# Kernel tuning notes

Hardware: AMD Instinct MI355X
Metric: run time of the kernel (lower is better)

## Reference

```python
import jax, jax.numpy as jnp
import numpy as np

KS = 3      # deform/standard conv kernel size
PAD = 1     # padding == dilation == 1
EPS = 1e-5  # BatchNorm eps


def conv2d(x, w, b, stride=1, padding=0):
    out = jax.lax.conv_general_dilated(
        x, w, (stride, stride), [(padding, padding), (padding, padding)],
        dimension_numbers=('NCHW', 'OIHW', 'NCHW'))
    return out + b[None, :, None, None]


def bn_relu(x, bn):
    gamma, beta, mean, var = bn[0], bn[1], bn[2], bn[3]
    inv = gamma / jnp.sqrt(var + EPS)
    y = x * inv[None, :, None, None] + (beta - mean * inv)[None, :, None, None]
    return jax.nn.relu(y)


def _gather(xp_flat, qx, qy, Wp, c):
    # xp_flat: (b, c, Hp*Wp); qx, qy: (b, h, w, N) int32 -> (b, c, h, w, N)
    b = qx.shape[0]
    idx = (qx * Wp + qy).reshape(b, 1, -1)
    out = jnp.take_along_axis(xp_flat, jnp.broadcast_to(idx, (b, c, idx.shape[-1])), axis=2)
    return out.reshape(b, c, *qx.shape[1:])


def deform_conv(x, w_off, b_off, w_def, b_def, stride=1):
    b, c, H, W = x.shape
    N = KS * KS
    offset = conv2d(x, w_off, b_off, stride=stride, padding=1)  # (b, 2N, h, w)
    h, w = offset.shape[2], offset.shape[3]
    xp = jnp.pad(x, ((0, 0), (0, 0), (PAD, PAD), (PAD, PAD)))
    Hp, Wp = H + 2 * PAD, W + 2 * PAD
    r = (KS - 1) // 2
    pn_x, pn_y = jnp.meshgrid(jnp.arange(-r, r + 1), jnp.arange(-r, r + 1), indexing='ij')
    p_n = jnp.concatenate([pn_x.ravel(), pn_y.ravel()]).astype(x.dtype)  # (2N,)
    p0_x = jnp.arange(1, h * stride + 1, stride, dtype=x.dtype)
    p0_y = jnp.arange(1, w * stride + 1, stride, dtype=x.dtype)
    p0 = jnp.concatenate([jnp.broadcast_to(p0_x[None, :, None], (N, h, w)),
                          jnp.broadcast_to(p0_y[None, None, :], (N, h, w))], 0)
    p = (offset + p_n[None, :, None, None] + p0[None]).transpose(0, 2, 3, 1)  # (b,h,w,2N)
    q = jnp.floor(jax.lax.stop_gradient(p))
    lt_x = jnp.clip(q[..., :N], 0, Hp - 1); lt_y = jnp.clip(q[..., N:], 0, Wp - 1)
    rb_x = jnp.clip(q[..., :N] + 1, 0, Hp - 1); rb_y = jnp.clip(q[..., N:] + 1, 0, Wp - 1)
    p_x = jnp.clip(p[..., :N], 0, Hp - 1); p_y = jnp.clip(p[..., N:], 0, Wp - 1)
    g_lt = (1 + (lt_x - p_x)) * (1 + (lt_y - p_y))
    g_rb = (1 - (rb_x - p_x)) * (1 - (rb_y - p_y))
    g_lb = (1 + (lt_x - p_x)) * (1 - (rb_y - p_y))
    g_rt = (1 - (rb_x - p_x)) * (1 + (lt_y - p_y))
    xpf = xp.reshape(b, c, -1)
    ii = lambda t: t.astype(jnp.int32)
    x_lt = _gather(xpf, ii(lt_x), ii(lt_y), Wp, c)
    x_rb = _gather(xpf, ii(rb_x), ii(rb_y), Wp, c)
    x_lb = _gather(xpf, ii(lt_x), ii(rb_y), Wp, c)
    x_rt = _gather(xpf, ii(rb_x), ii(lt_y), Wp, c)
    x_off = (g_lt[:, None] * x_lt + g_rb[:, None] * x_rb +
             g_lb[:, None] * x_lb + g_rt[:, None] * x_rt)  # (b, c, h, w, N)
    # (b,c,h,w,ks_i,ks_j) -> (b,c,h*ks,w*ks), N ordered row-major (i*ks+j)
    x_off = x_off.reshape(b, c, h, w, KS, KS).transpose(0, 1, 2, 4, 3, 5).reshape(b, c, h * KS, w * KS)
    return conv2d(x_off, w_def, b_def, stride=KS, padding=0)


def setup_inputs() -> dict:
    key = jax.random.key(0)
    ks = jax.random.split(key, 16)
    B, Cin, H, W = 4, 128, 96, 96
    C2, Cout = 128, 256
    s = 0.05
    bn = lambda k1, k2: jnp.stack([jnp.ones(C2, jnp.float32), jnp.zeros(C2, jnp.float32),
                                   jax.random.normal(k1, (C2,)) * 0.1,
                                   jax.random.uniform(k2, (C2,)) + 0.5])
    return {
        'x': jax.random.normal(ks[0], (B, Cin, H, W), jnp.float32),
        'w_in': jax.random.normal(ks[1], (C2, Cin, 1, 1)) * s,
        'b_in': jax.random.normal(ks[2], (C2,)) * s,
        'w_off': jax.random.normal(ks[3], (2 * KS * KS, C2, 3, 3)) * s,
        'b_off': jax.random.normal(ks[4], (2 * KS * KS,)) * s,
        'w_def': jax.random.normal(ks[5], (C2, C2, KS, KS)) * s,
        'b_def': jax.random.normal(ks[6], (C2,)) * s,
        'bn1': bn(ks[7], ks[8]),
        'w_std': jax.random.normal(ks[9], (C2, C2, 3, 3)) * s,
        'b_std': jax.random.normal(ks[10], (C2,)) * s,
        'bn2': bn(ks[11], ks[12]),
        'w_out': jax.random.normal(ks[13], (Cout, Cout, 1, 1)) * s,
        'b_out': jax.random.normal(ks[14], (Cout,)) * s,
    }


def reference(x, w_in, b_in, w_off, b_off, w_def, b_def, bn1, w_std, b_std, bn2, w_out, b_out):
    x_c = conv2d(x, w_in, b_in)                                    # 1x1 reduce to ch_out/2
    x1 = bn_relu(deform_conv(x_c, w_off, b_off, w_def, b_def), bn1)  # deformable branch
    x2 = bn_relu(conv2d(x_c, w_std, b_std, padding=1), bn2)       # standard 3x3 branch
    # stride == 1 path: concat(deform, std + residual) then 1x1 fuse
    return conv2d(jnp.concatenate([x1, x2 + x_c], axis=1), w_out, b_out)
```

## Files before the change

### kernel.cpp

```cpp
#include <hip/hip_runtime.h>
#include <hip/hip_bf16.h>

#define BB 4
#define CC 128
#define HH 96
#define WW 96
#define PX (HH*WW)
#define HP 98
#define WP 98
#define PP (HP*WP)
#define K2 1152
#define BN_EPS 1e-5f

typedef __hip_bfloat16 bf16;
typedef __attribute__((ext_vector_type(8))) short bf16x8;
typedef __attribute__((ext_vector_type(4))) float f32x4;
__device__ __forceinline__ float b2f(bf16 v) { return __bfloat162float(v); }
union F8 { bf16x8 v; bf16 h[8]; int4 i4; };

#define MFMA(a, b, c) __builtin_amdgcn_mfma_f32_16x16x32_bf16((a), (b), (c), 0, 0, 0)

__device__ __forceinline__ float ldin(const void* p, size_t i, int f) {
  return f ? ((const float*)p)[i] : b2f(((const bf16*)p)[i]);
}

#define P_BIN  0
#define P_BOFF 128
#define P_BDEF 160
#define P_BN1  288
#define P_BSTD 800
#define P_BN2  928
#define P_BOUT 1440

__global__ __launch_bounds__(256) void probe_params(
    const void* bn1, const void* b_in, const void* b_off, const void* b_def,
    const void* b_std, const void* bn2, const void* b_out,
    int* __restrict__ flag, float* __restrict__ prm) {
  int f = (((const unsigned*)bn1)[0] == 0x3F800000u) ? 1 : 0;
  if (threadIdx.x == 0) flag[0] = f;
  int t = threadIdx.x;
  if (t < 128) prm[P_BIN + t]  = ldin(b_in, t, f);
  if (t < 18)  prm[P_BOFF + t] = ldin(b_off, t, f);
  if (t < 128) prm[P_BDEF + t] = ldin(b_def, t, f);
  for (int i = t; i < 512; i += 256) prm[P_BN1 + i] = ldin(bn1, i, f);
  if (t < 128) prm[P_BSTD + t] = ldin(b_std, t, f);
  for (int i = t; i < 512; i += 256) prm[P_BN2 + i] = ldin(bn2, i, f);
  if (t < 256) prm[P_BOUT + t] = ldin(b_out, t, f);
}

__global__ __launch_bounds__(256) void prep_weights(
    const void* w_in, const void* w_def, const void* w_std, const void* w_out,
    const void* w_off,
    bf16* __restrict__ w_inB, bf16* __restrict__ w_defB,
    bf16* __restrict__ w_stdB, bf16* __restrict__ w_outB,
    bf16* __restrict__ w_offP, const int* __restrict__ flag) {
  int f = flag[0];
  int i = blockIdx.x * 256 + threadIdx.x;
  if (i < K2 * 128) {
    int o = i / K2, kk = i - o * K2;
    int c = kk / 9, n = kk - c * 9;
    int dst = o * K2 + n * 128 + c;
    w_defB[dst] = __float2bfloat16(ldin(w_def, i, f));
    w_stdB[dst] = __float2bfloat16(ldin(w_std, i, f));
  }
  if (i < 32 * K2) {
    int o = i / K2, kk = i - o * K2;
    int c = kk / 9, n = kk - c * 9;
    int dst = o * K2 + n * 128 + c;
    w_offP[dst] = (o < 18) ? __float2bfloat16(ldin(w_off, i, f))
                           : __float2bfloat16(0.f);
  }
  if (i < 128 * 128) w_inB[i]  = __float2bfloat16(ldin(w_in, i, f));
  if (i < 256 * 256) w_outB[i] = __float2bfloat16(ldin(w_out, i, f));
}

__global__ __launch_bounds__(256) void conv1x1_in(
    const void* __restrict__ x, const bf16* __restrict__ wB,
    const float* __restrict__ prm, bf16* __restrict__ xcT,
    const int* __restrict__ flag, int b0) {
  __shared__ bf16 ct[128][136];
  bf16 (*xt)[40] = (bf16(*)[40])ct;
  int f = flag[0];
  int tid = threadIdx.x;
  int p0 = blockIdx.x * 128;
  int bg = b0 + blockIdx.y, bl = blockIdx.y;
  int lane = tid & 63, wv = tid >> 6;
  int quad = lane >> 4, l16 = lane & 15;
  int krow = tid >> 3, pxs = (tid & 7) * 16;
  int sgrp = (tid & 7) & 3;
  f32x4 acc[2][8] = {};
  for (int k0 = 0; k0 < 128; k0 += 32) {
    union { bf16 h[16]; int4 i4[2]; } u;
    size_t base = (size_t)(bg * 128 + k0 + krow) * PX + p0 + pxs;
    if (f) {
      const float4* s = (const float4*)((const float*)x + base);
#pragma unroll
      for (int v = 0; v < 4; ++v) {
        float4 t = s[v];
        u.h[v * 4 + 0] = __float2bfloat16(t.x);
        u.h[v * 4 + 1] = __float2bfloat16(t.y);
        u.h[v * 4 + 2] = __float2bfloat16(t.z);
        u.h[v * 4 + 3] = __float2bfloat16(t.w);
      }
    } else {
      const int4* s = (const int4*)((const bf16*)x + base);
      u.i4[0] = s[0]; u.i4[1] = s[1];
    }
    int col = (((krow >> 3) ^ sgrp) << 3) | (krow & 7);
    __syncthreads();
#pragma unroll
    for (int j = 0; j < 16; ++j) xt[pxs + j][col] = u.h[j];
    __syncthreads();
    const bf16* wp = wB + (size_t)(wv * 32 + l16) * 128 + k0 + quad * 8;
    bf16x8 a0 = *(const bf16x8*)wp;
    bf16x8 a1 = *(const bf16x8*)(wp + 16 * 128);
#pragma unroll
    for (int p = 0; p < 8; ++p) {
      bf16x8 bfr = *(const bf16x8*)&xt[p * 16 + l16][(quad ^ (p & 3)) << 3];
      acc[0][p] = MFMA(a0, bfr, acc[0][p]);
      acc[1][p] = MFMA(a1, bfr, acc[1][p]);
    }
  }
  __syncthreads();
#pragma unroll
  for (int i = 0; i < 2; ++i)
#pragma unroll
    for (int r = 0; r < 4; ++r) {
      int o = wv * 32 + i * 16 + quad * 4 + r;
      float bs = prm[P_BIN + o];
#pragma unroll
      for (int p = 0; p < 8; ++p)
        ct[p * 16 + l16][o] = __float2bfloat16(acc[i][p][r] + bs);
    }
  __syncthreads();
  int px = tid >> 1, half = tid & 1;
  int gp = p0 + px;
  int h = gp / WW, w = gp - h * WW;
  bf16* dst = xcT + ((size_t)bl * PP + (size_t)(h + 1) * WP + (w + 1)) * CC + half * 64;
  const int4* src = (const int4*)&ct[px][half * 64];
#pragma unroll
  for (int j = 0; j < 8; ++j) ((int4*)dst)[j] = src[j];
}

__global__ __launch_bounds__(128) void conv_off_k(
    const bf16* __restrict__ xcT, const bf16* __restrict__ wP,
    const float* __restrict__ prm, float* __restrict__ off) {
  __shared__ bf16 xt[2][32][40];
  int tid = threadIdx.x;
  int p0 = blockIdx.x * 32;
  int bl = blockIdx.y;
  int lane = tid & 63, wv = tid >> 6;
  int quad = lane >> 4, l16 = lane & 15;
  int gpx = tid & 31, cq = tid >> 5;
  int gp = p0 + gpx;
  int gh = gp / WW, gw = gp - gh * WW;
  const bf16* xb = xcT + (size_t)bl * PP * CC;
  f32x4 acc[2] = {};
  int4 vc, vn;
  bf16x8 ac, an;
  vc = *(const int4*)(xb + ((size_t)gh * WP + gw) * CC + cq * 8);
  ac = *(const bf16x8*)(wP + (size_t)(wv * 16 + l16) * K2 + quad * 8);
  for (int ch = 0; ch < 36; ++ch) {
    if (ch + 1 < 36) {
      int ch1 = ch + 1;
      int n = ch1 >> 2, c0 = (ch1 & 3) << 5;
      int ti = n / 3, tj = n - ti * 3;
      vn = *(const int4*)(xb + ((size_t)(gh + ti) * WP + gw + tj) * CC + c0 + cq * 8);
      an = *(const bf16x8*)(wP + (size_t)(wv * 16 + l16) * K2 + n * 128 + c0 + quad * 8);
    }
    *(int4*)&xt[ch & 1][gpx][cq * 8] = vc;
    __syncthreads();
#pragma unroll
    for (int p = 0; p < 2; ++p) {
      bf16x8 bfr = *(const bf16x8*)&xt[ch & 1][p * 16 + l16][quad * 8];
      acc[p] = MFMA(ac, bfr, acc[p]);
    }
    vc = vn; ac = an;
  }
#pragma unroll
  for (int p = 0; p < 2; ++p) {
    int px = p0 + p * 16 + l16;
#pragma unroll
    for (int r = 0; r < 4; ++r) {
      int o = wv * 16 + quad * 4 + r;
      if (o < 18) off[((size_t)bl * 18 + o) * PX + px] = acc[p][r] + prm[P_BOFF + o];
    }
  }
}

__global__ __launch_bounds__(128) void deform_conv_k(
    const bf16* __restrict__ xcT, const float* __restrict__ off,
    const bf16* __restrict__ wB, const float* __restrict__ prm,
    bf16* __restrict__ ycat) {
  __shared__ int4   s_ofs[288];
  __shared__ float4 s_g[288];
  __shared__ bf16 xt[2][32][40];
  int tid = threadIdx.x;
  int p0 = blockIdx.x * 32;
  int bl = blockIdx.y;

  for (int it = tid; it < 288; it += 128) {
    int n = it >> 5, pl = it & 31;
    int p = p0 + pl;
    int h = p / WW, w = p - h * WW;
    float ox = off[(size_t)(bl * 18 + n) * PX + p];
    float oy = off[(size_t)(bl * 18 + 9 + n) * PX + p];
    float px = ox + (float)(n / 3 - 1) + (float)(h + 1);
    float py = oy + (float)(n % 3 - 1) + (float)(w + 1);
    float qx = floorf(px), qy = floorf(py);
    float ltx = fminf(fmaxf(qx, 0.f), (float)(HP - 1));
    float lty = fminf(fmaxf(qy, 0.f), (float)(WP - 1));
    float rbx = fminf(fmaxf(qx + 1.f, 0.f), (float)(HP - 1));
    float rby = fminf(fmaxf(qy + 1.f, 0.f), (float)(WP - 1));
    float pxc = fminf(fmaxf(px, 0.f), (float)(HP - 1));
    float pyc = fminf(fmaxf(py, 0.f), (float)(WP - 1));
    float ax = 1.f + (ltx - pxc), bx = 1.f - (rbx - pxc);
    float ay = 1.f + (lty - pyc), by = 1.f - (rby - pyc);
    int iltx = (int)ltx, ilty = (int)lty, irbx = (int)rbx, irby = (int)rby;
    s_ofs[it] = make_int4((iltx * WP + ilty) * (CC * 2), (irbx * WP + irby) * (CC * 2),
                          (iltx * WP + irby) * (CC * 2), (irbx * WP + ilty) * (CC * 2));
    s_g[it] = make_float4(ax * ay, bx * by, ax * by, bx * ay);
  }
  __syncthreads();

  int lane = tid & 63, wv = tid >> 6;
  int quad = lane >> 4, l16 = lane & 15;
  int gpx = tid & 31, cq = tid >> 5;
  const char* xbT = (const char*)(xcT + (size_t)bl * PP * CC);
  const bf16* wrow = wB + (size_t)(wv * 64 + l16) * K2 + quad * 8;
  f32x4 acc[4][2] = {};
  F8 Ac, Bc, Cc, Dc, An, Bn, Cn, Dn;
  float4 g4c, g4n;
  bf16x8 a_c[4], a_n[4];
  {
    int4 o4 = s_ofs[gpx];
    g4c = s_g[gpx];
    const char* cb = xbT + (size_t)(cq * 8) * 2;
    Ac.v = *(const bf16x8*)(cb + o4.x);
    Bc.v = *(const bf16x8*)(cb + o4.y);
    Cc.v = *(const bf16x8*)(cb + o4.z);
    Dc.v = *(const bf16x8*)(cb + o4.w);
#pragma unroll
    for (int s = 0; s < 4; ++s) a_c[s] = *(const bf16x8*)(wrow + (size_t)s * 16 * K2);
  }
  for (int ch = 0; ch < 36; ++ch) {
    if (ch + 1 < 36) {
      int ch1 = ch + 1;
      int n = ch1 >> 2, c0 = (ch1 & 3) << 5;
      int4 o4 = s_ofs[n * 32 + gpx];
      g4n = s_g[n * 32 + gpx];
      const char* cb = xbT + (size_t)(c0 + cq * 8) * 2;
      An.v = *(const bf16x8*)(cb + o4.x);
      Bn.v = *(const bf16x8*)(cb + o4.y);
      Cn.v = *(const bf16x8*)(cb + o4.z);
      Dn.v = *(const bf16x8*)(cb + o4.w);
#pragma unroll
      for (int s = 0; s < 4; ++s)
        a_n[s] = *(const bf16x8*)(wrow + n * 128 + c0 + (size_t)s * 16 * K2);
    }
    F8 u;
#pragma unroll
    for (int j = 0; j < 8; ++j) {
      float v = g4c.x * b2f(Ac.h[j]) + g4c.y * b2f(Bc.h[j]) +
                g4c.z * b2f(Cc.h[j]) + g4c.w * b2f(Dc.h[j]);
      u.h[j] = __float2bfloat16(v);
    }
    *(int4*)&xt[ch & 1][gpx][cq * 8] = u.i4;
    __syncthreads();
#pragma unroll
    for (int p = 0; p < 2; ++p) {
      bf16x8 bfr = *(const bf16x8*)&xt[ch & 1][p * 16 + l16][quad * 8];
#pragma unroll
      for (int s = 0; s < 4; ++s) acc[s][p] = MFMA(a_c[s], bfr, acc[s][p]);
    }
    Ac = An; Bc = Bn; Cc = Cn; Dc = Dn; g4c = g4n;
#pragma unroll
    for (int s = 0; s < 4; ++s) a_c[s] = a_n[s];
  }
#pragma unroll
  for (int s = 0; s < 4; ++s)
#pragma unroll
    for (int r = 0; r < 4; ++r) {
      int o = wv * 64 + s * 16 + quad * 4 + r;
      float bd = prm[P_BDEF + o];
      float g  = prm[P_BN1 + o],       be = prm[P_BN1 + 128 + o];
      float mn = prm[P_BN1 + 256 + o], vr = prm[P_BN1 + 384 + o];
      float inv = g / sqrtf(vr + BN_EPS);
      float add = be - mn * inv;
#pragma unroll
      for (int p = 0; p < 2; ++p) {
        int px = p0 + p * 16 + l16;
        float v = fmaxf((acc[s][p][r] + bd) * inv + add, 0.f);
        ycat[((size_t)bl * 256 + o) * PX + px] = __float2bfloat16(v);
      }
    }
}

__global__ __launch_bounds__(128) void std_conv_k(
    const bf16* __restrict__ xcT, const bf16* __restrict__ wB,
    const float* __restrict__ prm, bf16* __restrict__ ycat) {
  __shared__ bf16 xt[2][32][40];
  int tid = threadIdx.x;
  int p0 = blockIdx.x * 32;
  int bl = blockIdx.y;
  int lane = tid & 63, wv = tid >> 6;
  int quad = lane >> 4, l16 = lane & 15;
  int gpx = tid & 31, cq = tid >> 5;
  int gp = p0 + gpx;
  int gh = gp / WW, gw = gp - gh * WW;
  const bf16* xb = xcT + (size_t)bl * PP * CC;
  const bf16* wrow = wB + (size_t)(wv * 64 + l16) * K2 + quad * 8;
  f32x4 acc[4][2] = {};
  int4 vc, vn;
  bf16x8 a_c[4], a_n[4];
  vc = *(const int4*)(xb + ((size_t)gh * WP + gw) * CC + cq * 8);
#pragma unroll
  for (int s = 0; s < 4; ++s) a_c[s] = *(const bf16x8*)(wrow + (size_t)s * 16 * K2);
  for (int ch = 0; ch < 36; ++ch) {
    if (ch + 1 < 36) {
      int ch1 = ch + 1;
      int n = ch1 >> 2, c0 = (ch1 & 3) << 5;
      int ti = n / 3, tj = n - ti * 3;
      vn = *(const int4*)(xb + ((size_t)(gh + ti) * WP + gw + tj) * CC + c0 + cq * 8);
#pragma unroll
      for (int s = 0; s < 4; ++s)
        a_n[s] = *(const bf16x8*)(wrow + n * 128 + c0 + (size_t)s * 16 * K2);
    }
    *(int4*)&xt[ch & 1][gpx][cq * 8] = vc;
    __syncthreads();
#pragma unroll
    for (int p = 0; p < 2; ++p) {
      bf16x8 bfr = *(const bf16x8*)&xt[ch & 1][p * 16 + l16][quad * 8];
#pragma unroll
      for (int s = 0; s < 4; ++s) acc[s][p] = MFMA(a_c[s], bfr, acc[s][p]);
    }
    vc = vn;
#pragma unroll
    for (int s = 0; s < 4; ++s) a_c[s] = a_n[s];
  }
#pragma unroll
  for (int s = 0; s < 4; ++s)
#pragma unroll
    for (int r = 0; r < 4; ++r) {
      int o = wv * 64 + s * 16 + quad * 4 + r;
      float bs = prm[P_BSTD + o];
      float g  = prm[P_BN2 + o],       be = prm[P_BN2 + 128 + o];
      float mn = prm[P_BN2 + 256 + o], vr = prm[P_BN2 + 384 + o];
      float inv = g / sqrtf(vr + BN_EPS);
      float add = be - mn * inv;
#pragma unroll
      for (int p = 0; p < 2; ++p) {
        int px = p0 + p * 16 + l16;
        int hh = px / WW, ww = px - hh * WW;
        float res = b2f(xb[((size_t)(hh + 1) * WP + ww + 1) * CC + o]);
        float v = fmaxf((acc[s][p][r] + bs) * inv + add, 0.f) + res;
        ycat[((size_t)bl * 256 + 128 + o) * PX + px] = __float2bfloat16(v);
      }
    }
}

__global__ __launch_bounds__(256) void conv1x1_out(
    const bf16* __restrict__ ycat, const bf16* __restrict__ wB,
    const float* __restrict__ prm, void* __restrict__ out,
    const int* __restrict__ flag, int b0) {
  __shared__ bf16 xt[128][40];
  int f = flag[0];
  int tid = threadIdx.x;
  int p0 = blockIdx.x * 128;
  int half = blockIdx.y;
  int bg = b0 + blockIdx.z, bl = blockIdx.z;
  int lane = tid & 63, wv = tid >> 6;
  int quad = lane >> 4, l16 = lane & 15;
  int krow = tid >> 3, pxs = (tid & 7) * 16;
  int sgrp = (tid & 7) & 3;
  const bf16* yb = ycat + (size_t)bl * 256 * PX;
  f32x4 acc[2][8] = {};
  for (int k0 = 0; k0 < 256; k0 += 32) {
    union { bf16 h[16]; int4 i4[2]; } u;
    const int4* s = (const int4*)(yb + (size_t)(k0 + krow) * PX + p0 + pxs);
    u.i4[0] = s[0]; u.i4[1] = s[1];
    int col = (((krow >> 3) ^ sgrp) << 3) | (krow & 7);
    __syncthreads();
#pragma unroll
    for (int j = 0; j < 16; ++j) xt[pxs + j][col] = u.h[j];
    __syncthreads();
    const bf16* wp = wB + (size_t)(half * 128 + wv * 32 + l16) * 256 + k0 + quad * 8;
    bf16x8 a0 = *(const bf16x8*)wp;
    bf16x8 a1 = *(const bf16x8*)(wp + 16 * 256);
#pragma unroll
    for (int p = 0; p < 8; ++p) {
      bf16x8 bfr = *(const bf16x8*)&xt[p * 16 + l16][(quad ^ (p & 3)) << 3];
      acc[0][p] = MFMA(a0, bfr, acc[0][p]);
      acc[1][p] = MFMA(a1, bfr, acc[1][p]);
    }
  }
#pragma unroll
  for (int i = 0; i < 2; ++i)
#pragma unroll
    for (int r = 0; r < 4; ++r) {
      int o = half * 128 + wv * 32 + i * 16 + quad * 4 + r;
      float bs = prm[P_BOUT + o];
#pragma unroll
      for (int p = 0; p < 8; ++p) {
        int px = p0 + p * 16 + l16;
        size_t idx = ((size_t)bg * 256 + o) * PX + px;
        float v = acc[i][p][r] + bs;
        if (f) ((float*)out)[idx] = v;
        else   ((bf16*)out)[idx] = __float2bfloat16(v);
      }
    }
}

extern "C" void kernel_launch(void* const* d_in, const int* in_sizes, int n_in,
                              void* d_out, int out_size, void* d_ws, size_t ws_size,
                              hipStream_t stream) {
  const void* x     = d_in[0];
  const void* w_in  = d_in[1];
  const void* b_in  = d_in[2];
  const void* w_off = d_in[3];
  const void* b_off = d_in[4];
  const void* w_def = d_in[5];
  const void* b_def = d_in[6];
  const void* bn1   = d_in[7];
  const void* w_std = d_in[8];
  const void* b_std = d_in[9];
  const void* bn2   = d_in[10];
  const void* w_out = d_in[11];
  const void* b_out = d_in[12];

  char* wsb = (char*)d_ws;
  int*   flag   = (int*)wsb;
  float* prm    = (float*)(wsb + 1024);
  bf16*  w_offP = (bf16*)(wsb + 8192);
  bf16*  w_inB  = (bf16*)(wsb + 91136);
  bf16*  w_defB = (bf16*)(wsb + 123904);
  bf16*  w_stdB = (bf16*)(wsb + 418816);
  bf16*  w_outB = (bf16*)(wsb + 713728);
  const size_t FIXED = 847872;

  const size_t XCB  = (size_t)CC * PP * sizeof(bf16);
  const size_t OFFB = (size_t)18 * PX * sizeof(float);
  const size_t YCB  = (size_t)256 * PX * sizeof(bf16);
  const size_t PERB = XCB + OFFB + YCB;
  int nb = 1;
  if (ws_size > FIXED) {
    size_t fit = (ws_size - FIXED) / PERB;
    nb = (int)(fit < 1 ? 1 : (fit > BB ? BB : fit));
  }
  bf16*  xcA  = (bf16*)(wsb + FIXED);
  float* offA = (float*)(wsb + FIXED + (size_t)nb * XCB);
  bf16*  ycA  = (bf16*)(wsb + FIXED + (size_t)nb * (XCB + OFFB));

  probe_params<<<1, 256, 0, stream>>>(bn1, b_in, b_off, b_def, b_std, bn2, b_out,
                                      flag, prm);
  hipMemsetAsync(xcA, 0, (size_t)nb * XCB, stream);

  prep_weights<<<(K2 * 128 + 255) / 256, 256, 0, stream>>>(
      w_in, w_def, w_std, w_out, w_off, w_inB, w_defB, w_stdB, w_outB, w_offP, flag);

  for (int b0 = 0; b0 < BB; b0 += nb) {
    int nz = (BB - b0) < nb ? (BB - b0) : nb;
    conv1x1_in<<<dim3(PX / 128, nz), 256, 0, stream>>>(
        x, w_inB, prm, xcA, flag, b0);
    conv_off_k<<<dim3(PX / 32, nz), 128, 0, stream>>>(
        xcA, w_offP, prm, offA);
    deform_conv_k<<<dim3(PX / 32, nz), 128, 0, stream>>>(
        xcA, offA, w_defB, prm, ycA);
    std_conv_k<<<dim3(PX / 32, nz), 128, 0, stream>>>(
        xcA, w_stdB, prm, ycA);
    conv1x1_out<<<dim3(PX / 128, 2, nz), 256, 0, stream>>>(
        ycA, w_outB, prm, d_out, flag, b0);
  }
}
```

Baseline: 293.9 us.

## Split deform and std conv output channels across eight waves with full-channel K steps

The deformable and standard 3x3 conv kernels go from 128 to 512 threads per block. Each of the eight waves now owns 16 output channels instead of 64, and each loop step stages all 128 input channels of one tap, so the loop runs 9 steps instead of 36 and there are fewer barriers. More waves per 32-pixel tile should hide gather and weight-load latency better and cut per-thread accumulator registers. The cost is larger blocks with more threads waiting at each barrier, and the A-operand weight loads are now spread over more waves.

```diff
diff --git a/kernel.cpp b/kernel.cpp
--- a/kernel.cpp
+++ b/kernel.cpp
@@ -188,18 +188,18 @@
   }
 }
 
-__global__ __launch_bounds__(128) void deform_conv_k(
+__global__ __launch_bounds__(512) void deform_conv_k(
     const bf16* __restrict__ xcT, const float* __restrict__ off,
     const bf16* __restrict__ wB, const float* __restrict__ prm,
     bf16* __restrict__ ycat) {
   __shared__ int4   s_ofs[288];
   __shared__ float4 s_g[288];
-  __shared__ bf16 xt[2][32][40];
+  __shared__ bf16 xt[2][4][32][40];
   int tid = threadIdx.x;
   int p0 = blockIdx.x * 32;
   int bl = blockIdx.y;
 
-  for (int it = tid; it < 288; it += 128) {
+  for (int it = tid; it < 288; it += 512) {
     int n = it >> 5, pl = it & 31;
     int p = p0 + pl;
     int h = p / WW, w = p - h * WW;
@@ -225,38 +225,36 @@
 
   int lane = tid & 63, wv = tid >> 6;
   int quad = lane >> 4, l16 = lane & 15;
-  int gpx = tid & 31, cq = tid >> 5;
+  int oct = tid & 15, gpx = tid >> 4;
   const char* xbT = (const char*)(xcT + (size_t)bl * PP * CC);
-  const bf16* wrow = wB + (size_t)(wv * 64 + l16) * K2 + quad * 8;
-  f32x4 acc[4][2] = {};
+  const char* cb = xbT + oct * 16;
+  const bf16* wrow = wB + (size_t)(wv * 16 + l16) * K2 + quad * 8;
+  f32x4 acc[2] = {};
   F8 Ac, Bc, Cc, Dc, An, Bn, Cn, Dn;
   float4 g4c, g4n;
   bf16x8 a_c[4], a_n[4];
   {
     int4 o4 = s_ofs[gpx];
     g4c = s_g[gpx];
-    const char* cb = xbT + (size_t)(cq * 8) * 2;
     Ac.v = *(const bf16x8*)(cb + o4.x);
     Bc.v = *(const bf16x8*)(cb + o4.y);
     Cc.v = *(const bf16x8*)(cb + o4.z);
     Dc.v = *(const bf16x8*)(cb + o4.w);
 #pragma unroll
-    for (int s = 0; s < 4; ++s) a_c[s] = *(const bf16x8*)(wrow + (size_t)s * 16 * K2);
-  }
-  for (int ch = 0; ch < 36; ++ch) {
-    if (ch + 1 < 36) {
-      int ch1 = ch + 1;
-      int n = ch1 >> 2, c0 = (ch1 & 3) << 5;
-      int4 o4 = s_ofs[n * 32 + gpx];
-      g4n = s_g[n * 32 + gpx];
-      const char* cb = xbT + (size_t)(c0 + cq * 8) * 2;
+    for (int s = 0; s < 4; ++s) a_c[s] = *(const bf16x8*)(wrow + s * 32);
+  }
+  for (int r = 0; r < 9; ++r) {
+    if (r + 1 < 9) {
+      int m = (r + 1) * 32 + gpx;
+      int4 o4 = s_ofs[m];
+      g4n = s_g[m];
       An.v = *(const bf16x8*)(cb + o4.x);
       Bn.v = *(const bf16x8*)(cb + o4.y);
       Cn.v = *(const bf16x8*)(cb + o4.z);
       Dn.v = *(const bf16x8*)(cb + o4.w);
 #pragma unroll
       for (int s = 0; s < 4; ++s)
-        a_n[s] = *(const bf16x8*)(wrow + n * 128 + c0 + (size_t)s * 16 * K2);
+        a_n[s] = *(const bf16x8*)(wrow + (r + 1) * 128 + s * 32);
     }
     F8 u;
 #pragma unroll
@@ -265,98 +263,96 @@
                 g4c.z * b2f(Cc.h[j]) + g4c.w * b2f(Dc.h[j]);
       u.h[j] = __float2bfloat16(v);
     }
-    *(int4*)&xt[ch & 1][gpx][cq * 8] = u.i4;
-    __syncthreads();
+    *(int4*)&xt[r & 1][oct >> 2][gpx][(oct & 3) * 8] = u.i4;
+    __syncthreads();
+#pragma unroll
+    for (int c = 0; c < 4; ++c) {
+      bf16x8 b0 = *(const bf16x8*)&xt[r & 1][c][l16][quad * 8];
+      bf16x8 b1 = *(const bf16x8*)&xt[r & 1][c][16 + l16][quad * 8];
+      acc[0] = MFMA(a_c[c], b0, acc[0]);
+      acc[1] = MFMA(a_c[c], b1, acc[1]);
+    }
+    Ac = An; Bc = Bn; Cc = Cn; Dc = Dn; g4c = g4n;
+#pragma unroll
+    for (int s = 0; s < 4; ++s) a_c[s] = a_n[s];
+  }
+#pragma unroll
+  for (int r = 0; r < 4; ++r) {
+    int o = wv * 16 + quad * 4 + r;
+    float bd = prm[P_BDEF + o];
+    float g  = prm[P_BN1 + o],       be = prm[P_BN1 + 128 + o];
+    float mn = prm[P_BN1 + 256 + o], vr = prm[P_BN1 + 384 + o];
+    float inv = g / sqrtf(vr + BN_EPS);
+    float add = be - mn * inv;
 #pragma unroll
     for (int p = 0; p < 2; ++p) {
-      bf16x8 bfr = *(const bf16x8*)&xt[ch & 1][p * 16 + l16][quad * 8];
-#pragma unroll
-      for (int s = 0; s < 4; ++s) acc[s][p] = MFMA(a_c[s], bfr, acc[s][p]);
-    }
-    Ac = An; Bc = Bn; Cc = Cn; Dc = Dn; g4c = g4n;
-#pragma unroll
-    for (int s = 0; s < 4; ++s) a_c[s] = a_n[s];
-  }
-#pragma unroll
-  for (int s = 0; s < 4; ++s)
-#pragma unroll
-    for (int r = 0; r < 4; ++r) {
-      int o = wv * 64 + s * 16 + quad * 4 + r;
-      float bd = prm[P_BDEF + o];
-      float g  = prm[P_BN1 + o],       be = prm[P_BN1 + 128 + o];
-      float mn = prm[P_BN1 + 256 + o], vr = prm[P_BN1 + 384 + o];
-      float inv = g / sqrtf(vr + BN_EPS);
-      float add = be - mn * inv;
-#pragma unroll
-      for (int p = 0; p < 2; ++p) {
-        int px = p0 + p * 16 + l16;
-        float v = fmaxf((acc[s][p][r] + bd) * inv + add, 0.f);
-        ycat[((size_t)bl * 256 + o) * PX + px] = __float2bfloat16(v);
-      }
-    }
-}
-
-__global__ __launch_bounds__(128) void std_conv_k(
+      int px = p0 + p * 16 + l16;
+      float v = fmaxf((acc[p][r] + bd) * inv + add, 0.f);
+      ycat[((size_t)bl * 256 + o) * PX + px] = __float2bfloat16(v);
+    }
+  }
+}
+
+__global__ __launch_bounds__(512) void std_conv_k(
     const bf16* __restrict__ xcT, const bf16* __restrict__ wB,
     const float* __restrict__ prm, bf16* __restrict__ ycat) {
-  __shared__ bf16 xt[2][32][40];
+  __shared__ bf16 xt[2][4][32][40];
   int tid = threadIdx.x;
   int p0 = blockIdx.x * 32;
   int bl = blockIdx.y;
   int lane = tid & 63, wv = tid >> 6;
   int quad = lane >> 4, l16 = lane & 15;
-  int gpx = tid & 31, cq = tid >> 5;
+  int oct = tid & 15, gpx = tid >> 4;
   int gp = p0 + gpx;
   int gh = gp / WW, gw = gp - gh * WW;
   const bf16* xb = xcT + (size_t)bl * PP * CC;
-  const bf16* wrow = wB + (size_t)(wv * 64 + l16) * K2 + quad * 8;
-  f32x4 acc[4][2] = {};
+  const bf16* xpx = xb + ((size_t)gh * WP + gw) * CC + oct * 8;
+  const bf16* wrow = wB + (size_t)(wv * 16 + l16) * K2 + quad * 8;
+  f32x4 acc[2] = {};
   int4 vc, vn;
   bf16x8 a_c[4], a_n[4];
-  vc = *(const int4*)(xb + ((size_t)gh * WP + gw) * CC + cq * 8);
-#pragma unroll
-  for (int s = 0; s < 4; ++s) a_c[s] = *(const bf16x8*)(wrow + (size_t)s * 16 * K2);
-  for (int ch = 0; ch < 36; ++ch) {
-    if (ch + 1 < 36) {
-      int ch1 = ch + 1;
-      int n = ch1 >> 2, c0 = (ch1 & 3) << 5;
+  vc = *(const int4*)xpx;
+#pragma unroll
+  for (int s = 0; s < 4; ++s) a_c[s] = *(const bf16x8*)(wrow + s * 32);
+  for (int r = 0; r < 9; ++r) {
+    if (r + 1 < 9) {
+      int n = r + 1;
       int ti = n / 3, tj = n - ti * 3;
-      vn = *(const int4*)(xb + ((size_t)(gh + ti) * WP + gw + tj) * CC + c0 + cq * 8);
+      vn = *(const int4*)(xpx + ((size_t)ti * WP + tj) * CC);
 #pragma unroll
       for (int s = 0; s < 4; ++s)
-        a_n[s] = *(const bf16x8*)(wrow + n * 128 + c0 + (size_t)s * 16 * K2);
-    }
-    *(int4*)&xt[ch & 1][gpx][cq * 8] = vc;
-    __syncthreads();
+        a_n[s] = *(const bf16x8*)(wrow + (r + 1) * 128 + s * 32);
+    }
+    *(int4*)&xt[r & 1][oct >> 2][gpx][(oct & 3) * 8] = vc;
+    __syncthreads();
+#pragma unroll
+    for (int c = 0; c < 4; ++c) {
+      bf16x8 b0 = *(const bf16x8*)&xt[r & 1][c][l16][quad * 8];
+      bf16x8 b1 = *(const bf16x8*)&xt[r & 1][c][16 + l16][quad * 8];
+      acc[0] = MFMA(a_c[c], b0, acc[0]);
+      acc[1] = MFMA(a_c[c], b1, acc[1]);
+    }
+    vc = vn;
+#pragma unroll
+    for (int s = 0; s < 4; ++s) a_c[s] = a_n[s];
+  }
+#pragma unroll
+  for (int r = 0; r < 4; ++r) {
+    int o = wv * 16 + quad * 4 + r;
+    float bs = prm[P_BSTD + o];
+    float g  = prm[P_BN2 + o],       be = prm[P_BN2 + 128 + o];
+    float mn = prm[P_BN2 + 256 + o], vr = prm[P_BN2 + 384 + o];
+    float inv = g / sqrtf(vr + BN_EPS);
+    float add = be - mn * inv;
 #pragma unroll
     for (int p = 0; p < 2; ++p) {
-      bf16x8 bfr = *(const bf16x8*)&xt[ch & 1][p * 16 + l16][quad * 8];
-#pragma unroll
-      for (int s = 0; s < 4; ++s) acc[s][p] = MFMA(a_c[s], bfr, acc[s][p]);
-    }
-    vc = vn;
-#pragma unroll
-    for (int s = 0; s < 4; ++s) a_c[s] = a_n[s];
-  }
-#pragma unroll
-  for (int s = 0; s < 4; ++s)
-#pragma unroll
-    for (int r = 0; r < 4; ++r) {
-      int o = wv * 64 + s * 16 + quad * 4 + r;
-      float bs = prm[P_BSTD + o];
-      float g  = prm[P_BN2 + o],       be = prm[P_BN2 + 128 + o];
-      float mn = prm[P_BN2 + 256 + o], vr = prm[P_BN2 + 384 + o];
-      float inv = g / sqrtf(vr + BN_EPS);
-      float add = be - mn * inv;
-#pragma unroll
-      for (int p = 0; p < 2; ++p) {
-        int px = p0 + p * 16 + l16;
-        int hh = px / WW, ww = px - hh * WW;
-        float res = b2f(xb[((size_t)(hh + 1) * WP + ww + 1) * CC + o]);
-        float v = fmaxf((acc[s][p][r] + bs) * inv + add, 0.f) + res;
-        ycat[((size_t)bl * 256 + 128 + o) * PX + px] = __float2bfloat16(v);
-      }
-    }
+      int px = p0 + p * 16 + l16;
+      int hh = px / WW, ww = px - hh * WW;
+      float res = b2f(xb[((size_t)(hh + 1) * WP + ww + 1) * CC + o]);
+      float v = fmaxf((acc[p][r] + bs) * inv + add, 0.f) + res;
+      ycat[((size_t)bl * 256 + 128 + o) * PX + px] = __float2bfloat16(v);
+    }
+  }
 }
 
 __global__ __launch_bounds__(256) void conv1x1_out(
@@ -464,9 +460,9 @@
         x, w_inB, prm, xcA, flag, b0);
     conv_off_k<<<dim3(PX / 32, nz), 128, 0, stream>>>(
         xcA, w_offP, prm, offA);
-    deform_conv_k<<<dim3(PX / 32, nz), 128, 0, stream>>>(
+    deform_conv_k<<<dim3(PX / 32, nz), 512, 0, stream>>>(
         xcA, offA, w_defB, prm, ycA);
-    std_conv_k<<<dim3(PX / 32, nz), 128, 0, stream>>>(
+    std_conv_k<<<dim3(PX / 32, nz), 512, 0, stream>>>(
         xcA, w_stdB, prm, ycA);
     conv1x1_out<<<dim3(PX / 128, 2, nz), 256, 0, stream>>>(
         ycA, w_outB, prm, d_out, flag, b0);
```

Result: faster. 255.4 us (-13.1%).
